# Performance work log

Measured on AMD Instinct MI355X. Metric: run time of the kernel, lower is better.

The kernel has to match this reference:

```python
import jax, jax.numpy as jnp
import numpy as np

B, N, M = 1024, 512, 256  # batch, n_locations, vec_size
EPS_ADD = 1e-16   # additive eps used by the torch module
EPS_COS = 1e-8    # torch.cosine_similarity default eps (clamps norms)


def setup_inputs() -> dict:
    key0 = jax.random.key(0)
    ks = jax.random.split(key0, 9)
    return {
        "memory": jax.random.normal(ks[0], (B, N, M), jnp.float32),
        "key":    jax.random.normal(ks[1], (B, M), jnp.float32),
        "beta":   jax.random.uniform(ks[2], (B, 1), jnp.float32),
        "g":      jax.random.uniform(ks[3], (B, 1), jnp.float32),
        "s":      jax.random.uniform(ks[4], (B, 3), jnp.float32),
        "gamma":  jax.random.uniform(ks[5], (B, 1), jnp.float32),
        "w_prev": jax.random.uniform(ks[6], (B, N), jnp.float32),
        "e":      jax.random.uniform(ks[7], (B, M), jnp.float32),
        "a":      jax.random.normal(ks[8], (B, M), jnp.float32),
    }


def reference(memory, key, beta, g, s, gamma, w_prev, e, a):
    b, n, m = memory.shape
    # --- content addressing: cosine similarity of each memory row vs key ---
    mem = memory + EPS_ADD
    k = key[:, None, :] + EPS_ADD                       # [B,1,M]
    num = jnp.sum(mem * k, axis=-1)                     # [B,N]
    den = (jnp.maximum(jnp.linalg.norm(mem, axis=-1), EPS_COS)
           * jnp.maximum(jnp.linalg.norm(k, axis=-1), EPS_COS))
    w_c = jax.nn.softmax(beta * (num / den), axis=1)    # [B,N]
    # --- interpolation gate ---
    w_g = g * w_c + (1.0 - g) * w_prev                  # [B,N]
    # --- circular convolutional shift (kernel size 3, cross-correlation) ---
    # torch: t = [w_g[-1], w_g, w_g[0]]; out[i] = sum_j t[i+j]*s[j]
    #       = sum_{d in {-1,0,1}} w_g[(i+d) mod N] * s[d+1]
    idx = (jnp.arange(n)[:, None] + jnp.arange(-1, 2)[None, :]) % n  # [N,3]
    w_tilda = jnp.einsum('bnk,bk->bn', w_g[:, idx], s)  # [B,N]
    # --- sharpening ---
    w_pow = w_tilda ** gamma                            # gamma [B,1] broadcasts
    w = w_pow / (jnp.sum(w_pow, axis=1, keepdims=True) + EPS_ADD)
    # --- read ---
    r = jnp.einsum('bn,bnm->bm', w, memory)             # [B,M]
    # --- write (erase + add via outer products) ---
    erase = w[:, :, None] * e[:, None, :]               # [B,N,M]
    add = w[:, :, None] * a[:, None, :]                 # [B,N,M]
    new_mem = memory * (1.0 - erase) + add              # [B,N,M]
    # flatten all outputs into one array: [B, N + M + N*M]
    return jnp.concatenate([w, r, new_mem.reshape(b, n * m)], axis=1)
```

## Files before the change

### kernel.cpp

```cpp
#include <hip/hip_runtime.h>
#include <math.h>

#define BB 1024
#define NN 512
#define MM 256
#define OUTROW (NN + MM + NN * MM)
#define EPS_ADD 1e-16f
#define EPS_COS 1e-8f
#define G_REG 11
#define G_TOT 16

typedef float f4v __attribute__((ext_vector_type(4)));

__device__ inline float waveReduceSum(float v) {
#pragma unroll
    for (int off = 32; off > 0; off >>= 1) v += __shfl_xor(v, off);
    return v;
}

__device__ __forceinline__ void ldgrp(f4v (&buf)[4], const float* __restrict__ rp) {
#pragma unroll
    for (int mc = 0; mc < 4; ++mc)
        buf[mc] = *reinterpret_cast<const f4v*>(rp + mc * 64);
}
__device__ __forceinline__ void ldgrp_nt(f4v (&buf)[4], const float* __restrict__ rp) {
#pragma unroll
    for (int mc = 0; mc < 4; ++mc)
        buf[mc] = __builtin_nontemporal_load(reinterpret_cast<const f4v*>(rp + mc * 64));
}

__device__ __forceinline__ void redgrp(const f4v (&buf)[4], const f4v (&kf)[4],
                                       float bet, float kn, float* __restrict__ sc,
                                       int row, int sl) {
    float dot = 0.f, ssq = 0.f;
#pragma unroll
    for (int mc = 0; mc < 4; ++mc) {
        const float mx = buf[mc].x + EPS_ADD, my = buf[mc].y + EPS_ADD;
        const float mz = buf[mc].z + EPS_ADD, mw = buf[mc].w + EPS_ADD;
        dot += mx * kf[mc].x + my * kf[mc].y + mz * kf[mc].z + mw * kf[mc].w;
        ssq += mx * mx + my * my + mz * mz + mw * mw;
    }
#pragma unroll
    for (int off = 8; off > 0; off >>= 1) {
        dot += __shfl_xor(dot, off);
        ssq += __shfl_xor(ssq, off);
    }
    if (sl == 0)
        sc[row] = bet * dot / (fmaxf(sqrtf(ssq), EPS_COS) * kn);
}

__device__ __forceinline__ void procgrp(const f4v (&mvv)[4], float wn,
                                        const f4v (&ev)[4], const f4v (&av)[4],
                                        f4v (&acc)[4], float* __restrict__ op) {
#pragma unroll
    for (int mc = 0; mc < 4; ++mc) {
        const f4v nm = mvv[mc] * (1.f - wn * ev[mc]) + wn * av[mc];
        __builtin_nontemporal_store(nm, reinterpret_cast<f4v*>(op + mc * 64));
        acc[mc] += wn * mvv[mc];
    }
}

__global__ __launch_bounds__(512, 2) void ntm_memory_kernel(
    const float* __restrict__ memory, const float* __restrict__ key,
    const float* __restrict__ beta, const float* __restrict__ g,
    const float* __restrict__ s, const float* __restrict__ gamma,
    const float* __restrict__ w_prev, const float* __restrict__ e,
    const float* __restrict__ a, float* __restrict__ out) {
    const int b    = blockIdx.x;
    const int t    = threadIdx.x;
    const int lane = t & 63;
    const int wave = t >> 6;
    const int sub  = lane >> 4;
    const int sl   = lane & 15;

    __shared__ float key_lds[MM];
    __shared__ float sc[NN];
    __shared__ float wg[NN];
    __shared__ float wf[NN];
    __shared__ float ea_lds[2 * MM];
    __shared__ float red[8];
    __shared__ float rpart[8][MM];

    const float* __restrict__ memb = memory + (size_t)b * NN * MM;
    float* __restrict__ outb       = out + (size_t)b * OUTROW;

    if (t < MM) {
        key_lds[t]      = key[b * MM + t] + EPS_ADD;
        ea_lds[MM + t]  = a[b * MM + t];
    } else {
        const int i = t - MM;
        ea_lds[i] = e[b * MM + i];
    }
    __syncthreads();

    if (t < MM) {
        float kv = key_lds[t];
        float ss = waveReduceSum(kv * kv);
        if (lane == 0) red[wave] = ss;
    }
    __syncthreads();
    const float kn  = fmaxf(sqrtf(red[0] + red[1] + red[2] + red[3]), EPS_COS);
    const float bet = beta[b];
    const float gv  = g[b];
    const float gam = gamma[b];
    const float s0  = s[b * 3 + 0];
    const float s1  = s[b * 3 + 1];
    const float s2  = s[b * 3 + 2];
    __syncthreads();

    const int rowbase = wave * 64 + sub;
    const float* __restrict__ rp0 = memb + (size_t)rowbase * MM + sl * 4;

    f4v kf[4];
#pragma unroll
    for (int mc = 0; mc < 4; ++mc)
        kf[mc] = *reinterpret_cast<const f4v*>(&key_lds[mc * 64 + sl * 4]);

    f4v tile[G_REG][4];
#pragma unroll
    for (int gp = 0; gp < G_REG; ++gp)
        ldgrp_nt(tile[gp], rp0 + (size_t)(4 * gp) * MM);

#pragma unroll
    for (int gp = 0; gp < G_REG; ++gp)
        redgrp(tile[gp], kf, bet, kn, sc, rowbase + 4 * gp, sl);

    {
        f4v sA[4], sB[4];
        ldgrp(sA, rp0 + (size_t)(4 * (G_REG + 0)) * MM);
        ldgrp(sB, rp0 + (size_t)(4 * (G_REG + 1)) * MM);
        redgrp(sA, kf, bet, kn, sc, rowbase + 4 * (G_REG + 0), sl);
        ldgrp(sA, rp0 + (size_t)(4 * (G_REG + 2)) * MM);
        redgrp(sB, kf, bet, kn, sc, rowbase + 4 * (G_REG + 1), sl);
        ldgrp(sB, rp0 + (size_t)(4 * (G_REG + 3)) * MM);
        redgrp(sA, kf, bet, kn, sc, rowbase + 4 * (G_REG + 2), sl);
        ldgrp(sA, rp0 + (size_t)(4 * (G_REG + 4)) * MM);
        redgrp(sB, kf, bet, kn, sc, rowbase + 4 * (G_REG + 3), sl);
        redgrp(sA, kf, bet, kn, sc, rowbase + 4 * (G_REG + 4), sl);
    }
    __syncthreads();

    const float v  = sc[t];
    const float ex = __expf(v);
    {
        const float s1w = waveReduceSum(ex);
        if (lane == 0) red[wave] = s1w;
    }
    __syncthreads();
    float esum = 0.f;
#pragma unroll
    for (int k = 0; k < 8; k++) esum += red[k];
    const float w_c = ex / esum;

    wg[t] = gv * w_c + (1.f - gv) * w_prev[b * NN + t];
    __syncthreads();
    const float wt = wg[(t + NN - 1) & (NN - 1)] * s0 + wg[t] * s1 +
                     wg[(t + 1) & (NN - 1)] * s2;
    const float wp = __powf(wt, gam);
    {
        const float sw = waveReduceSum(wp);
        if (lane == 0) red[wave] = sw;
    }
    __syncthreads();
    float wsum = 0.f;
#pragma unroll
    for (int k = 0; k < 8; k++) wsum += red[k];
    const float wv = wp / (wsum + EPS_ADD);
    wf[t]   = wv;
    outb[t] = wv;

    f4v ev[4], av[4], acc[4];
#pragma unroll
    for (int mc = 0; mc < 4; ++mc) {
        ev[mc]  = *reinterpret_cast<const f4v*>(&ea_lds[mc * 64 + sl * 4]);
        av[mc]  = *reinterpret_cast<const f4v*>(&ea_lds[MM + mc * 64 + sl * 4]);
        acc[mc] = (f4v)0.f;
    }
    float* __restrict__ ob0 = outb + (NN + MM) + (size_t)rowbase * MM + sl * 4;

#pragma unroll
    for (int gp = 0; gp < G_REG; ++gp)
        procgrp(tile[gp], wf[rowbase + 4 * gp], ev, av, acc,
                ob0 + (size_t)(4 * gp) * MM);

    {
        f4v sA[4], sB[4];
        ldgrp(sA, rp0 + (size_t)(4 * (G_REG + 0)) * MM);
        ldgrp(sB, rp0 + (size_t)(4 * (G_REG + 1)) * MM);
        procgrp(sA, wf[rowbase + 4 * (G_REG + 0)], ev, av, acc,
                ob0 + (size_t)(4 * (G_REG + 0)) * MM);
        ldgrp(sA, rp0 + (size_t)(4 * (G_REG + 2)) * MM);
        procgrp(sB, wf[rowbase + 4 * (G_REG + 1)], ev, av, acc,
                ob0 + (size_t)(4 * (G_REG + 1)) * MM);
        ldgrp(sB, rp0 + (size_t)(4 * (G_REG + 3)) * MM);
        procgrp(sA, wf[rowbase + 4 * (G_REG + 2)], ev, av, acc,
                ob0 + (size_t)(4 * (G_REG + 2)) * MM);
        ldgrp(sA, rp0 + (size_t)(4 * (G_REG + 4)) * MM);
        procgrp(sB, wf[rowbase + 4 * (G_REG + 3)], ev, av, acc,
                ob0 + (size_t)(4 * (G_REG + 3)) * MM);
        procgrp(sA, wf[rowbase + 4 * (G_REG + 4)], ev, av, acc,
                ob0 + (size_t)(4 * (G_REG + 4)) * MM);
    }

#pragma unroll
    for (int mc = 0; mc < 4; ++mc) {
        acc[mc].x += __shfl_xor(acc[mc].x, 16); acc[mc].y += __shfl_xor(acc[mc].y, 16);
        acc[mc].z += __shfl_xor(acc[mc].z, 16); acc[mc].w += __shfl_xor(acc[mc].w, 16);
        acc[mc].x += __shfl_xor(acc[mc].x, 32); acc[mc].y += __shfl_xor(acc[mc].y, 32);
        acc[mc].z += __shfl_xor(acc[mc].z, 32); acc[mc].w += __shfl_xor(acc[mc].w, 32);
    }
    if (sub == 0) {
#pragma unroll
        for (int mc = 0; mc < 4; ++mc)
            *reinterpret_cast<f4v*>(&rpart[wave][mc * 64 + sl * 4]) = acc[mc];
    }
    __syncthreads();
    if (t < MM) {
        float rsum = 0.f;
#pragma unroll
        for (int k = 0; k < 8; k++) rsum += rpart[k][t];
        outb[NN + t] = rsum;
    }
}

extern "C" void kernel_launch(void* const* d_in, const int* in_sizes, int n_in,
                              void* d_out, int out_size, void* d_ws, size_t ws_size,
                              hipStream_t stream) {
    const float* memory = (const float*)d_in[0];
    const float* key    = (const float*)d_in[1];
    const float* beta   = (const float*)d_in[2];
    const float* g      = (const float*)d_in[3];
    const float* s      = (const float*)d_in[4];
    const float* gamma  = (const float*)d_in[5];
    const float* w_prev = (const float*)d_in[6];
    const float* e      = (const float*)d_in[7];
    const float* a      = (const float*)d_in[8];
    float* out = (float*)d_out;

    ntm_memory_kernel<<<BB, 512, 0, stream>>>(memory, key, beta, g, s, gamma,
                                              w_prev, e, a, out);
}
```

Before: 208.0 us.

## Halve block size to 256 threads with each wave covering 128 rows

Switches to 256 threads per block, so each wave handles 128 memory rows instead of 64. Only 11 row groups stay register-resident and the other 21 are streamed twice through a double buffer, once for scoring and once for the write. The softmax and sharpen stages now process two elements per thread. This adds work per thread and rereads about two thirds of the memory tile from global memory or cache, rather than a third as before. In exchange the block has fewer threads and fewer barriers and reduction partials.

```diff
diff --git a/kernel.cpp b/kernel.cpp
--- a/kernel.cpp
+++ b/kernel.cpp
@@ -8,7 +8,8 @@
 #define EPS_ADD 1e-16f
 #define EPS_COS 1e-8f
 #define G_REG 11
-#define G_TOT 16
+#define G_STREAM 21
+#define G_TOT 32
 
 typedef float f4v __attribute__((ext_vector_type(4)));
 
@@ -60,7 +61,7 @@
     }
 }
 
-__global__ __launch_bounds__(512, 2) void ntm_memory_kernel(
+__global__ __launch_bounds__(256, 2) void ntm_memory_kernel(
     const float* __restrict__ memory, const float* __restrict__ key,
     const float* __restrict__ beta, const float* __restrict__ g,
     const float* __restrict__ s, const float* __restrict__ gamma,
@@ -78,24 +79,20 @@
     __shared__ float wg[NN];
     __shared__ float wf[NN];
     __shared__ float ea_lds[2 * MM];
-    __shared__ float red[8];
-    __shared__ float rpart[8][MM];
+    __shared__ float red[4];
+    __shared__ float rpart[4][MM];
 
     const float* __restrict__ memb = memory + (size_t)b * NN * MM;
     float* __restrict__ outb       = out + (size_t)b * OUTROW;
 
-    if (t < MM) {
-        key_lds[t]      = key[b * MM + t] + EPS_ADD;
-        ea_lds[MM + t]  = a[b * MM + t];
-    } else {
-        const int i = t - MM;
-        ea_lds[i] = e[b * MM + i];
-    }
-    __syncthreads();
-
-    if (t < MM) {
-        float kv = key_lds[t];
-        float ss = waveReduceSum(kv * kv);
+    key_lds[t]     = key[b * MM + t] + EPS_ADD;
+    ea_lds[t]      = e[b * MM + t];
+    ea_lds[MM + t] = a[b * MM + t];
+    __syncthreads();
+
+    {
+        const float kv = key_lds[t];
+        const float ss = waveReduceSum(kv * kv);
         if (lane == 0) red[wave] = ss;
     }
     __syncthreads();
@@ -106,9 +103,8 @@
     const float s0  = s[b * 3 + 0];
     const float s1  = s[b * 3 + 1];
     const float s2  = s[b * 3 + 2];
-    __syncthreads();
-
-    const int rowbase = wave * 64 + sub;
+
+    const int rowbase = wave * 128 + sub;
     const float* __restrict__ rp0 = memb + (size_t)rowbase * MM + sl * 4;
 
     f4v kf[4];
@@ -126,48 +122,53 @@
         redgrp(tile[gp], kf, bet, kn, sc, rowbase + 4 * gp, sl);
 
     {
-        f4v sA[4], sB[4];
-        ldgrp(sA, rp0 + (size_t)(4 * (G_REG + 0)) * MM);
-        ldgrp(sB, rp0 + (size_t)(4 * (G_REG + 1)) * MM);
-        redgrp(sA, kf, bet, kn, sc, rowbase + 4 * (G_REG + 0), sl);
-        ldgrp(sA, rp0 + (size_t)(4 * (G_REG + 2)) * MM);
-        redgrp(sB, kf, bet, kn, sc, rowbase + 4 * (G_REG + 1), sl);
-        ldgrp(sB, rp0 + (size_t)(4 * (G_REG + 3)) * MM);
-        redgrp(sA, kf, bet, kn, sc, rowbase + 4 * (G_REG + 2), sl);
-        ldgrp(sA, rp0 + (size_t)(4 * (G_REG + 4)) * MM);
-        redgrp(sB, kf, bet, kn, sc, rowbase + 4 * (G_REG + 3), sl);
-        redgrp(sA, kf, bet, kn, sc, rowbase + 4 * (G_REG + 4), sl);
-    }
-    __syncthreads();
-
-    const float v  = sc[t];
-    const float ex = __expf(v);
-    {
-        const float s1w = waveReduceSum(ex);
+        f4v s0b[4], s1b[4];
+        ldgrp(s0b, rp0 + (size_t)(4 * (G_REG + 0)) * MM);
+        ldgrp(s1b, rp0 + (size_t)(4 * (G_REG + 1)) * MM);
+#pragma unroll
+        for (int j = 0; j < G_STREAM; ++j) {
+            if ((j & 1) == 0) {
+                redgrp(s0b, kf, bet, kn, sc, rowbase + 4 * (G_REG + j), sl);
+                if (j + 2 < G_STREAM)
+                    ldgrp(s0b, rp0 + (size_t)(4 * (G_REG + j + 2)) * MM);
+            } else {
+                redgrp(s1b, kf, bet, kn, sc, rowbase + 4 * (G_REG + j), sl);
+                if (j + 2 < G_STREAM)
+                    ldgrp(s1b, rp0 + (size_t)(4 * (G_REG + j + 2)) * MM);
+            }
+        }
+    }
+    __syncthreads();
+
+    const float v0 = sc[t], v1 = sc[t + 256];
+    const float ex0 = __expf(v0), ex1 = __expf(v1);
+    {
+        const float s1w = waveReduceSum(ex0 + ex1);
         if (lane == 0) red[wave] = s1w;
     }
     __syncthreads();
-    float esum = 0.f;
-#pragma unroll
-    for (int k = 0; k < 8; k++) esum += red[k];
-    const float w_c = ex / esum;
-
-    wg[t] = gv * w_c + (1.f - gv) * w_prev[b * NN + t];
-    __syncthreads();
-    const float wt = wg[(t + NN - 1) & (NN - 1)] * s0 + wg[t] * s1 +
-                     wg[(t + 1) & (NN - 1)] * s2;
-    const float wp = __powf(wt, gam);
-    {
-        const float sw = waveReduceSum(wp);
+    const float esum = red[0] + red[1] + red[2] + red[3];
+
+    wg[t]       = gv * (ex0 / esum) + (1.f - gv) * w_prev[b * NN + t];
+    wg[t + 256] = gv * (ex1 / esum) + (1.f - gv) * w_prev[b * NN + t + 256];
+    __syncthreads();
+    const float wt0 = wg[(t + NN - 1) & (NN - 1)] * s0 + wg[t] * s1 +
+                      wg[(t + 1) & (NN - 1)] * s2;
+    const float wt1 = wg[(t + 255) & (NN - 1)] * s0 + wg[t + 256] * s1 +
+                      wg[(t + 257) & (NN - 1)] * s2;
+    const float wp0 = __powf(wt0, gam), wp1 = __powf(wt1, gam);
+    {
+        const float sw = waveReduceSum(wp0 + wp1);
         if (lane == 0) red[wave] = sw;
     }
     __syncthreads();
-    float wsum = 0.f;
-#pragma unroll
-    for (int k = 0; k < 8; k++) wsum += red[k];
-    const float wv = wp / (wsum + EPS_ADD);
-    wf[t]   = wv;
-    outb[t] = wv;
+    const float wsum = red[0] + red[1] + red[2] + red[3] + EPS_ADD;
+    const float wv0 = wp0 / wsum, wv1 = wp1 / wsum;
+    wf[t]         = wv0;
+    wf[t + 256]   = wv1;
+    outb[t]       = wv0;
+    outb[t + 256] = wv1;
+    __syncthreads();
 
     f4v ev[4], av[4], acc[4];
 #pragma unroll
@@ -178,28 +179,28 @@
     }
     float* __restrict__ ob0 = outb + (NN + MM) + (size_t)rowbase * MM + sl * 4;
 
+    f4v s0b[4], s1b[4];
+    ldgrp(s0b, rp0 + (size_t)(4 * (G_REG + 0)) * MM);
+    ldgrp(s1b, rp0 + (size_t)(4 * (G_REG + 1)) * MM);
+
 #pragma unroll
     for (int gp = 0; gp < G_REG; ++gp)
         procgrp(tile[gp], wf[rowbase + 4 * gp], ev, av, acc,
                 ob0 + (size_t)(4 * gp) * MM);
 
-    {
-        f4v sA[4], sB[4];
-        ldgrp(sA, rp0 + (size_t)(4 * (G_REG + 0)) * MM);
-        ldgrp(sB, rp0 + (size_t)(4 * (G_REG + 1)) * MM);
-        procgrp(sA, wf[rowbase + 4 * (G_REG + 0)], ev, av, acc,
-                ob0 + (size_t)(4 * (G_REG + 0)) * MM);
-        ldgrp(sA, rp0 + (size_t)(4 * (G_REG + 2)) * MM);
-        procgrp(sB, wf[rowbase + 4 * (G_REG + 1)], ev, av, acc,
-                ob0 + (size_t)(4 * (G_REG + 1)) * MM);
-        ldgrp(sB, rp0 + (size_t)(4 * (G_REG + 3)) * MM);
-        procgrp(sA, wf[rowbase + 4 * (G_REG + 2)], ev, av, acc,
-                ob0 + (size_t)(4 * (G_REG + 2)) * MM);
-        ldgrp(sA, rp0 + (size_t)(4 * (G_REG + 4)) * MM);
-        procgrp(sB, wf[rowbase + 4 * (G_REG + 3)], ev, av, acc,
-                ob0 + (size_t)(4 * (G_REG + 3)) * MM);
-        procgrp(sA, wf[rowbase + 4 * (G_REG + 4)], ev, av, acc,
-                ob0 + (size_t)(4 * (G_REG + 4)) * MM);
+#pragma unroll
+    for (int j = 0; j < G_STREAM; ++j) {
+        if ((j & 1) == 0) {
+            procgrp(s0b, wf[rowbase + 4 * (G_REG + j)], ev, av, acc,
+                    ob0 + (size_t)(4 * (G_REG + j)) * MM);
+            if (j + 2 < G_STREAM)
+                ldgrp(s0b, rp0 + (size_t)(4 * (G_REG + j + 2)) * MM);
+        } else {
+            procgrp(s1b, wf[rowbase + 4 * (G_REG + j)], ev, av, acc,
+                    ob0 + (size_t)(4 * (G_REG + j)) * MM);
+            if (j + 2 < G_STREAM)
+                ldgrp(s1b, rp0 + (size_t)(4 * (G_REG + j + 2)) * MM);
+        }
     }
 
 #pragma unroll
@@ -215,12 +216,7 @@
             *reinterpret_cast<f4v*>(&rpart[wave][mc * 64 + sl * 4]) = acc[mc];
     }
     __syncthreads();
-    if (t < MM) {
-        float rsum = 0.f;
-#pragma unroll
-        for (int k = 0; k < 8; k++) rsum += rpart[k][t];
-        outb[NN + t] = rsum;
-    }
+    outb[NN + t] = rpart[0][t] + rpart[1][t] + rpart[2][t] + rpart[3][t];
 }
 
 extern "C" void kernel_launch(void* const* d_in, const int* in_sizes, int n_in,
@@ -237,6 +233,6 @@
     const float* a      = (const float*)d_in[8];
     float* out = (float*)d_out;
 
-    ntm_memory_kernel<<<BB, 512, 0, stream>>>(memory, key, beta, g, s, gamma,
+    ntm_memory_kernel<<<BB, 256, 0, stream>>>(memory, key, beta, g, s, gamma,
                                               w_prev, e, a, out);
 }
```

Result: slower. 298.1 us (+43.3%).

## Shrink register-resident tile to raise occupancy and stream remaining rows twice

Applied to the files above, without the earlier changes.

Cuts the number of memory row-groups held in registers from 11 to 4 and streams the other 12 with double buffering, re-reading them from global memory in the write phase. The e/a vectors are now read from LDS per group instead of being kept in registers, and launch bounds ask for 4 blocks per CU instead of 2. The aim is higher occupancy to hide memory latency, at the cost of re-reading about three quarters of each batch's memory slice (possibly from L2) and extra LDS traffic.

```diff
diff --git a/kernel.cpp b/kernel.cpp
--- a/kernel.cpp
+++ b/kernel.cpp
@@ -7,7 +7,8 @@
 #define OUTROW (NN + MM + NN * MM)
 #define EPS_ADD 1e-16f
 #define EPS_COS 1e-8f
-#define G_REG 11
+#define G_REG 4
+#define G_STREAM 12
 #define G_TOT 16
 
 typedef float f4v __attribute__((ext_vector_type(4)));
@@ -49,18 +50,20 @@
         sc[row] = bet * dot / (fmaxf(sqrtf(ssq), EPS_COS) * kn);
 }
 
-__device__ __forceinline__ void procgrp(const f4v (&mvv)[4], float wn,
-                                        const f4v (&ev)[4], const f4v (&av)[4],
-                                        f4v (&acc)[4], float* __restrict__ op) {
+__device__ __forceinline__ void procgrp_lds(const f4v (&mvv)[4], float wn,
+                                            const float* __restrict__ ea,
+                                            f4v (&acc)[4], float* __restrict__ op) {
 #pragma unroll
     for (int mc = 0; mc < 4; ++mc) {
-        const f4v nm = mvv[mc] * (1.f - wn * ev[mc]) + wn * av[mc];
+        const f4v ev = *reinterpret_cast<const f4v*>(ea + mc * 64);
+        const f4v av = *reinterpret_cast<const f4v*>(ea + MM + mc * 64);
+        const f4v nm = mvv[mc] * (1.f - wn * ev) + wn * av;
         __builtin_nontemporal_store(nm, reinterpret_cast<f4v*>(op + mc * 64));
         acc[mc] += wn * mvv[mc];
     }
 }
 
-__global__ __launch_bounds__(512, 2) void ntm_memory_kernel(
+__global__ __launch_bounds__(512, 4) void ntm_memory_kernel(
     const float* __restrict__ memory, const float* __restrict__ key,
     const float* __restrict__ beta, const float* __restrict__ g,
     const float* __restrict__ s, const float* __restrict__ gamma,
@@ -121,22 +124,25 @@
     for (int gp = 0; gp < G_REG; ++gp)
         ldgrp_nt(tile[gp], rp0 + (size_t)(4 * gp) * MM);
 
+    f4v sA[4], sB[4];
+    ldgrp(sA, rp0 + (size_t)(4 * (G_REG + 0)) * MM);
+    ldgrp(sB, rp0 + (size_t)(4 * (G_REG + 1)) * MM);
+
 #pragma unroll
     for (int gp = 0; gp < G_REG; ++gp)
         redgrp(tile[gp], kf, bet, kn, sc, rowbase + 4 * gp, sl);
 
-    {
-        f4v sA[4], sB[4];
-        ldgrp(sA, rp0 + (size_t)(4 * (G_REG + 0)) * MM);
-        ldgrp(sB, rp0 + (size_t)(4 * (G_REG + 1)) * MM);
-        redgrp(sA, kf, bet, kn, sc, rowbase + 4 * (G_REG + 0), sl);
-        ldgrp(sA, rp0 + (size_t)(4 * (G_REG + 2)) * MM);
-        redgrp(sB, kf, bet, kn, sc, rowbase + 4 * (G_REG + 1), sl);
-        ldgrp(sB, rp0 + (size_t)(4 * (G_REG + 3)) * MM);
-        redgrp(sA, kf, bet, kn, sc, rowbase + 4 * (G_REG + 2), sl);
-        ldgrp(sA, rp0 + (size_t)(4 * (G_REG + 4)) * MM);
-        redgrp(sB, kf, bet, kn, sc, rowbase + 4 * (G_REG + 3), sl);
-        redgrp(sA, kf, bet, kn, sc, rowbase + 4 * (G_REG + 4), sl);
+#pragma unroll
+    for (int j = 0; j < G_STREAM; ++j) {
+        if ((j & 1) == 0) {
+            redgrp(sA, kf, bet, kn, sc, rowbase + 4 * (G_REG + j), sl);
+            if (j + 2 < G_STREAM)
+                ldgrp(sA, rp0 + (size_t)(4 * (G_REG + j + 2)) * MM);
+        } else {
+            redgrp(sB, kf, bet, kn, sc, rowbase + 4 * (G_REG + j), sl);
+            if (j + 2 < G_STREAM)
+                ldgrp(sB, rp0 + (size_t)(4 * (G_REG + j + 2)) * MM);
+        }
     }
     __syncthreads();
 
@@ -169,37 +175,33 @@
     wf[t]   = wv;
     outb[t] = wv;
 
-    f4v ev[4], av[4], acc[4];
-#pragma unroll
-    for (int mc = 0; mc < 4; ++mc) {
-        ev[mc]  = *reinterpret_cast<const f4v*>(&ea_lds[mc * 64 + sl * 4]);
-        av[mc]  = *reinterpret_cast<const f4v*>(&ea_lds[MM + mc * 64 + sl * 4]);
-        acc[mc] = (f4v)0.f;
-    }
+    f4v acc[4];
+#pragma unroll
+    for (int mc = 0; mc < 4; ++mc) acc[mc] = (f4v)0.f;
+    const float* __restrict__ eap = &ea_lds[sl * 4];
     float* __restrict__ ob0 = outb + (NN + MM) + (size_t)rowbase * MM + sl * 4;
 
+    ldgrp(sA, rp0 + (size_t)(4 * (G_REG + 0)) * MM);
+    ldgrp(sB, rp0 + (size_t)(4 * (G_REG + 1)) * MM);
+
 #pragma unroll
     for (int gp = 0; gp < G_REG; ++gp)
-        procgrp(tile[gp], wf[rowbase + 4 * gp], ev, av, acc,
-                ob0 + (size_t)(4 * gp) * MM);
-
-    {
-        f4v sA[4], sB[4];
-        ldgrp(sA, rp0 + (size_t)(4 * (G_REG + 0)) * MM);
-        ldgrp(sB, rp0 + (size_t)(4 * (G_REG + 1)) * MM);
-        procgrp(sA, wf[rowbase + 4 * (G_REG + 0)], ev, av, acc,
-                ob0 + (size_t)(4 * (G_REG + 0)) * MM);
-        ldgrp(sA, rp0 + (size_t)(4 * (G_REG + 2)) * MM);
-        procgrp(sB, wf[rowbase + 4 * (G_REG + 1)], ev, av, acc,
-                ob0 + (size_t)(4 * (G_REG + 1)) * MM);
-        ldgrp(sB, rp0 + (size_t)(4 * (G_REG + 3)) * MM);
-        procgrp(sA, wf[rowbase + 4 * (G_REG + 2)], ev, av, acc,
-                ob0 + (size_t)(4 * (G_REG + 2)) * MM);
-        ldgrp(sA, rp0 + (size_t)(4 * (G_REG + 4)) * MM);
-        procgrp(sB, wf[rowbase + 4 * (G_REG + 3)], ev, av, acc,
-                ob0 + (size_t)(4 * (G_REG + 3)) * MM);
-        procgrp(sA, wf[rowbase + 4 * (G_REG + 4)], ev, av, acc,
-                ob0 + (size_t)(4 * (G_REG + 4)) * MM);
+        procgrp_lds(tile[gp], wf[rowbase + 4 * gp], eap, acc,
+                    ob0 + (size_t)(4 * gp) * MM);
+
+#pragma unroll
+    for (int j = 0; j < G_STREAM; ++j) {
+        if ((j & 1) == 0) {
+            procgrp_lds(sA, wf[rowbase + 4 * (G_REG + j)], eap, acc,
+                        ob0 + (size_t)(4 * (G_REG + j)) * MM);
+            if (j + 2 < G_STREAM)
+                ldgrp(sA, rp0 + (size_t)(4 * (G_REG + j + 2)) * MM);
+        } else {
+            procgrp_lds(sB, wf[rowbase + 4 * (G_REG + j)], eap, acc,
+                        ob0 + (size_t)(4 * (G_REG + j)) * MM);
+            if (j + 2 < G_STREAM)
+                ldgrp(sB, rp0 + (size_t)(4 * (G_REG + j + 2)) * MM);
+        }
     }
 
 #pragma unroll
```

Measured after the change: 354.7 us. +70.5%, slower.

## Stage memory rows in LDS via async global_load_lds to avoid re-reading

Applied to the files above, without the earlier changes.

During the content-addressing pass, each wave issues asynchronous global-to-LDS copies of four of its five streamed row groups into a new 128KB shared buffer. The write/read pass then takes those rows from LDS instead of reloading them from global memory, and only one group is still fetched from global. The aim is to cut the second pass's global read traffic and hide its latency behind the softmax and sharpening phases. The large LDS footprint likely limits the kernel to one 512-thread block per CU instead of the two the launch bounds target, which reduces latency hiding.

```diff
diff --git a/kernel.cpp b/kernel.cpp
--- a/kernel.cpp
+++ b/kernel.cpp
@@ -8,6 +8,7 @@
 #define EPS_ADD 1e-16f
 #define EPS_COS 1e-8f
 #define G_REG 11
+#define G_LDS 4
 #define G_TOT 16
 
 typedef float f4v __attribute__((ext_vector_type(4)));
@@ -80,6 +81,7 @@
     __shared__ float ea_lds[2 * MM];
     __shared__ float red[8];
     __shared__ float rpart[8][MM];
+    __shared__ float TL[8 * G_LDS * 4 * MM];
 
     const float* __restrict__ memb = memory + (size_t)b * NN * MM;
     float* __restrict__ outb       = out + (size_t)b * OUTROW;
@@ -138,6 +140,21 @@
         redgrp(sB, kf, bet, kn, sc, rowbase + 4 * (G_REG + 3), sl);
         redgrp(sA, kf, bet, kn, sc, rowbase + 4 * (G_REG + 4), sl);
     }
+
+    {
+#pragma unroll
+        for (int gl = 0; gl < G_LDS; ++gl) {
+#pragma unroll
+            for (int rr = 0; rr < 4; ++rr) {
+                const int ldsrow = (wave * G_LDS + gl) * 4 + rr;
+                const float* src = memb + (size_t)(wave * 64 + 4 * (G_REG + gl) + rr) * MM + lane * 4;
+                __builtin_amdgcn_global_load_lds(
+                    (const __attribute__((address_space(1))) void*)src,
+                    (__attribute__((address_space(3))) void*)&TL[ldsrow * MM],
+                    16, 0, 0);
+            }
+        }
+    }
     __syncthreads();
 
     const float v  = sc[t];
@@ -169,6 +186,8 @@
     wf[t]   = wv;
     outb[t] = wv;
 
+    asm volatile("s_waitcnt vmcnt(0)" ::: "memory");
+
     f4v ev[4], av[4], acc[4];
 #pragma unroll
     for (int mc = 0; mc < 4; ++mc) {
@@ -178,29 +197,26 @@
     }
     float* __restrict__ ob0 = outb + (NN + MM) + (size_t)rowbase * MM + sl * 4;
 
+    f4v sS[4];
+    ldgrp(sS, rp0 + (size_t)(4 * (G_REG + G_LDS)) * MM);
+
 #pragma unroll
     for (int gp = 0; gp < G_REG; ++gp)
         procgrp(tile[gp], wf[rowbase + 4 * gp], ev, av, acc,
                 ob0 + (size_t)(4 * gp) * MM);
 
-    {
-        f4v sA[4], sB[4];
-        ldgrp(sA, rp0 + (size_t)(4 * (G_REG + 0)) * MM);
-        ldgrp(sB, rp0 + (size_t)(4 * (G_REG + 1)) * MM);
-        procgrp(sA, wf[rowbase + 4 * (G_REG + 0)], ev, av, acc,
-                ob0 + (size_t)(4 * (G_REG + 0)) * MM);
-        ldgrp(sA, rp0 + (size_t)(4 * (G_REG + 2)) * MM);
-        procgrp(sB, wf[rowbase + 4 * (G_REG + 1)], ev, av, acc,
-                ob0 + (size_t)(4 * (G_REG + 1)) * MM);
-        ldgrp(sB, rp0 + (size_t)(4 * (G_REG + 3)) * MM);
-        procgrp(sA, wf[rowbase + 4 * (G_REG + 2)], ev, av, acc,
-                ob0 + (size_t)(4 * (G_REG + 2)) * MM);
-        ldgrp(sA, rp0 + (size_t)(4 * (G_REG + 4)) * MM);
-        procgrp(sB, wf[rowbase + 4 * (G_REG + 3)], ev, av, acc,
-                ob0 + (size_t)(4 * (G_REG + 3)) * MM);
-        procgrp(sA, wf[rowbase + 4 * (G_REG + 4)], ev, av, acc,
-                ob0 + (size_t)(4 * (G_REG + 4)) * MM);
-    }
+#pragma unroll
+    for (int gl = 0; gl < G_LDS; ++gl) {
+        const float* TLrow = &TL[((wave * G_LDS + gl) * 4 + sub) * MM];
+        f4v bufL[4];
+#pragma unroll
+        for (int mc = 0; mc < 4; ++mc)
+            bufL[mc] = *reinterpret_cast<const f4v*>(TLrow + mc * 64 + sl * 4);
+        procgrp(bufL, wf[rowbase + 4 * (G_REG + gl)], ev, av, acc,
+                ob0 + (size_t)(4 * (G_REG + gl)) * MM);
+    }
+    procgrp(sS, wf[rowbase + 4 * (G_REG + G_LDS)], ev, av, acc,
+            ob0 + (size_t)(4 * (G_REG + G_LDS)) * MM);
 
 #pragma unroll
     for (int mc = 0; mc < 4; ++mc) {
```

New measurement: 206.1 us. Within noise of the previous version (-0.9%).
